# Optimization experiments

Hardware: AMD Instinct MI355X
Metric: run time of the kernel (lower is better)

## Reference

```python
import jax, jax.numpy as jnp
import numpy as np

E = 1_000_000
C_IN = 11
H = 64
N_LAYERS = 4
LN_EPS = 1e-5


def setup_inputs() -> dict:
    key = jax.random.key(0)
    ks = jax.random.split(key, 12)
    x = jax.random.normal(ks[0], (E, C_IN), dtype=jnp.float32)
    neighbors = jax.random.randint(ks[1], (E, 4), 0, E)
    s0 = 1.0 / np.sqrt(5 * C_IN)
    s1 = 1.0 / np.sqrt(5 * H)
    w0 = jax.random.uniform(ks[2], (5 * C_IN, H), jnp.float32, -s0, s0)
    b0 = jax.random.uniform(ks[3], (H,), jnp.float32, -s0, s0)
    w_rest = jax.random.uniform(ks[4], (N_LAYERS - 1, 5 * H, H), jnp.float32, -s1, s1)
    b_rest = jax.random.uniform(ks[5], (N_LAYERS - 1, H), jnp.float32, -s1, s1)
    ln_g = jnp.ones((N_LAYERS, H), jnp.float32)
    ln_b = jnp.zeros((N_LAYERS, H), jnp.float32)
    sc1 = 1.0 / np.sqrt(H)
    sc2 = 1.0 / np.sqrt(H // 2)
    cw1 = jax.random.uniform(ks[6], (H, H // 2), jnp.float32, -sc1, sc1)
    cb1 = jax.random.uniform(ks[7], (H // 2,), jnp.float32, -sc1, sc1)
    cw2 = jax.random.uniform(ks[8], (H // 2, 1), jnp.float32, -sc2, sc2)
    cb2 = jax.random.uniform(ks[9], (1,), jnp.float32, -sc2, sc2)
    return {"x": x, "neighbors": neighbors, "w0": w0, "b0": b0,
            "w_rest": w_rest, "b_rest": b_rest, "ln_g": ln_g, "ln_b": ln_b,
            "cw1": cw1, "cb1": cb1, "cw2": cw2, "cb2": cb2}


def _mesh_conv(x, neighbors, W, b):
    # Gather 4-ring neighbor features: [E,4,C]
    n = x[neighbors]
    a, bb, c, d = n[:, 0], n[:, 1], n[:, 2], n[:, 3]
    # Symmetric MeshCNN features -> 5*C, then linear projection.
    feats = jnp.concatenate([x, jnp.abs(a - c), a + c, jnp.abs(bb - d), bb + d], axis=-1)
    return feats @ W + b


def _layernorm(h, g, b):
    mu = jnp.mean(h, axis=-1, keepdims=True)
    var = jnp.var(h, axis=-1, keepdims=True)
    return (h - mu) * jax.lax.rsqrt(var + LN_EPS) * g + b


def reference(x, neighbors, w0, b0, w_rest, b_rest, ln_g, ln_b, cw1, cb1, cw2, cb2):
    # Layer 0 (no residual; dropout is identity in eval mode)
    h = jax.nn.relu(_layernorm(_mesh_conv(x, neighbors, w0, b0), ln_g[0], ln_b[0]))
    x = h
    for i in range(1, N_LAYERS):
        h = _mesh_conv(x, neighbors, w_rest[i - 1], b_rest[i - 1])
        h = jax.nn.relu(_layernorm(h, ln_g[i], ln_b[i]))
        x = h + x  # residual from layer 2 onward (shapes match)
    z = jax.nn.relu(x @ cw1 + cb1)
    logits = (z @ cw2 + cb2).squeeze(-1)
    return logits
```

## Files before the change

kernel.cpp:

```cpp
#include <hip/hip_runtime.h>
#include <hip/hip_bf16.h>
#include <math.h>

#define E_EDGES 1000000
#define LN_EPS  1e-5f

typedef unsigned short u16;
typedef __bf16 bf16x8 __attribute__((ext_vector_type(8)));
typedef float  f32x16 __attribute__((ext_vector_type(16)));

__device__ __forceinline__ float lo2f(unsigned d) {
    union { unsigned u; float f; } v; v.u = d << 16; return v.f;
}
__device__ __forceinline__ float hi2f(unsigned d) {
    union { unsigned u; float f; } v; v.u = d & 0xffff0000u; return v.f;
}
__device__ __forceinline__ unsigned pk2(float lo, float hi) {
    __hip_bfloat162 h = __float22bfloat162_rn(make_float2(lo, hi));
    unsigned r; __builtin_memcpy(&r, &h, 4); return r;
}

__global__ __launch_bounds__(256) void wconv_kernel(
    const float* __restrict__ wr, const float* __restrict__ w0,
    u16* __restrict__ wf)
{
    const int s = blockIdx.x * 256 + threadIdx.x;
    const int l    = s & 63;
    const int nt   = (s >> 6) & 1;
    const int col  = nt * 32 + (l & 31);
    const int half = l >> 5;
    uint4 pk;
    if (s < 3 * 2560) {
        const int L  = s / 2560;
        const int sl = s % 2560;
        const int kb = (sl >> 7) * 16 + half * 8;
        const float* W = wr + L * 320 * 64;
        pk.x = pk2(W[(kb+0)*64+col], W[(kb+1)*64+col]);
        pk.y = pk2(W[(kb+2)*64+col], W[(kb+3)*64+col]);
        pk.z = pk2(W[(kb+4)*64+col], W[(kb+5)*64+col]);
        pk.w = pk2(W[(kb+6)*64+col], W[(kb+7)*64+col]);
    } else {
        const int sl = s - 3 * 2560;
        const int kb = (sl >> 7) * 16 + half * 8;
        float v[8];
        #pragma unroll
        for (int p = 0; p < 8; ++p) v[p] = (kb + p < 55) ? w0[(kb+p)*64 + col] : 0.f;
        pk.x = pk2(v[0],v[1]); pk.y = pk2(v[2],v[3]);
        pk.z = pk2(v[4],v[5]); pk.w = pk2(v[6],v[7]);
    }
    *(uint4*)&wf[(size_t)s * 8] = pk;
}

__global__ __launch_bounds__(256, 4) void layer_mfma(
    const u16* __restrict__ xin, const int* __restrict__ nbr,
    const u16* __restrict__ wf, const float* __restrict__ bias,
    const float* __restrict__ lng, const float* __restrict__ lnb,
    u16* __restrict__ xout)
{
    __shared__ u16 afrag[2 * 20 * 64 * 8];
    const int t  = threadIdx.x;
    const int l  = t & 63;
    const int wv = t >> 6;
    const int e0 = blockIdx.x * 64;

    {
        const int el = t >> 2;
        const int cq = t & 3;
        const size_t e = (size_t)(e0 + el);
        const int4 n = *(const int4*)(nbr + 4 * e);
        const u16* xr = xin + e * 64           + cq * 16;
        const u16* ar = xin + (size_t)n.x * 64 + cq * 16;
        const u16* br = xin + (size_t)n.y * 64 + cq * 16;
        const u16* cr = xin + (size_t)n.z * 64 + cq * 16;
        const u16* dr = xin + (size_t)n.w * 64 + cq * 16;
        const uint4 xv0 = *(const uint4*)(xr);     const uint4 xv1 = *(const uint4*)(xr + 8);
        const uint4 av0 = *(const uint4*)(ar);     const uint4 av1 = *(const uint4*)(ar + 8);
        const uint4 bv0 = *(const uint4*)(br);     const uint4 bv1 = *(const uint4*)(br + 8);
        const uint4 cv0 = *(const uint4*)(cr);     const uint4 cv1 = *(const uint4*)(cr + 8);
        const uint4 dv0 = *(const uint4*)(dr);     const uint4 dv1 = *(const uint4*)(dr + 8);
        const int mt    = el >> 5;
        const int lane0 = el & 31;
        u16* abase = afrag + (size_t)mt * (20 * 64 * 8);
        #pragma unroll
        for (int w8 = 0; w8 < 2; ++w8) {
            const uint4 xv = w8 ? xv1 : xv0;
            const uint4 av = w8 ? av1 : av0;
            const uint4 bv = w8 ? bv1 : bv0;
            const uint4 cv = w8 ? cv1 : cv0;
            const uint4 dv = w8 ? dv1 : dv0;
            const int ldst = lane0 + 32 * w8;
            uint4 g1, g2, g3, g4;
            const unsigned* ap = (const unsigned*)&av;
            const unsigned* bp = (const unsigned*)&bv;
            const unsigned* cp = (const unsigned*)&cv;
            const unsigned* dp = (const unsigned*)&dv;
            unsigned* g1p = (unsigned*)&g1; unsigned* g2p = (unsigned*)&g2;
            unsigned* g3p = (unsigned*)&g3; unsigned* g4p = (unsigned*)&g4;
            #pragma unroll
            for (int i = 0; i < 4; ++i) {
                const float a0 = lo2f(ap[i]), a1 = hi2f(ap[i]);
                const float c0 = lo2f(cp[i]), c1 = hi2f(cp[i]);
                g1p[i] = pk2(fabsf(a0 - c0), fabsf(a1 - c1));
                g2p[i] = pk2(a0 + c0, a1 + c1);
                const float b0 = lo2f(bp[i]), b1 = hi2f(bp[i]);
                const float d0 = lo2f(dp[i]), d1 = hi2f(dp[i]);
                g3p[i] = pk2(fabsf(b0 - d0), fabsf(b1 - d1));
                g4p[i] = pk2(b0 + d0, b1 + d1);
            }
            *(uint4*)(abase + (size_t)(((0*4 + cq) * 64) + ldst) * 8) = xv;
            *(uint4*)(abase + (size_t)(((1*4 + cq) * 64) + ldst) * 8) = g1;
            *(uint4*)(abase + (size_t)(((2*4 + cq) * 64) + ldst) * 8) = g2;
            *(uint4*)(abase + (size_t)(((3*4 + cq) * 64) + ldst) * 8) = g3;
            *(uint4*)(abase + (size_t)(((4*4 + cq) * 64) + ldst) * 8) = g4;
        }
    }
    __syncthreads();

    const int mt = wv >> 1, nt = wv & 1;
    f32x16 acc = {};
    const u16* ab = afrag + (size_t)mt * (20 * 64 * 8) + l * 8;
    const u16* bb = wf + (size_t)(nt * 64 + l) * 8;
    #pragma unroll
    for (int ks = 0; ks < 20; ++ks) {
        const bf16x8 a8 = *(const bf16x8*)(ab + ks * 512);
        const bf16x8 b8 = *(const bf16x8*)(bb + ks * 1024);
        acc = __builtin_amdgcn_mfma_f32_32x32x16_bf16(a8, b8, acc, 0, 0, 0);
    }
    __syncthreads();

    float* ebuf = (float*)afrag;
    {
        const int col  = nt * 32 + (l & 31);
        const int quad = l >> 5;
        const float bc = bias[col];
        #pragma unroll
        for (int r = 0; r < 16; ++r) {
            const int row = mt * 32 + (r & 3) + 8 * (r >> 2) + 4 * quad;
            ebuf[row * 68 + col] = acc[r] + bc;
        }
    }
    __syncthreads();

    {
        const int el = t >> 2, q = t & 3;
        const float* rp = ebuf + el * 68 + q * 16;
        float v[16];
        float s = 0.f, qs = 0.f;
        #pragma unroll
        for (int i = 0; i < 16; ++i) { v[i] = rp[i]; s += v[i]; qs += v[i] * v[i]; }
        s  += __shfl_xor(s, 1);  s  += __shfl_xor(s, 2);
        qs += __shfl_xor(qs, 1); qs += __shfl_xor(qs, 2);
        const float mu   = s * (1.f / 64.f);
        const float var  = qs * (1.f / 64.f) - mu * mu;
        const float rinv = rsqrtf(var + LN_EPS);
        const size_t e   = (size_t)(e0 + el);
        const u16* resp  = xin + e * 64 + q * 16;
        u16* outp        = xout + e * 64 + q * 16;
        #pragma unroll
        for (int h = 0; h < 2; ++h) {
            const uint4 res = *(const uint4*)(resp + h * 8);
            const unsigned* rr = (const unsigned*)&res;
            uint4 o; unsigned* op = (unsigned*)&o;
            #pragma unroll
            for (int i = 0; i < 4; ++i) {
                const int ci = q * 16 + h * 8 + i * 2;
                const float y0 = fmaxf(fmaf((v[h*8 + i*2]     - mu) * rinv, lng[ci],     lnb[ci]),     0.f) + lo2f(rr[i]);
                const float y1 = fmaxf(fmaf((v[h*8 + i*2 + 1] - mu) * rinv, lng[ci + 1], lnb[ci + 1]), 0.f) + hi2f(rr[i]);
                op[i] = pk2(y0, y1);
            }
            *(uint4*)(outp + h * 8) = o;
        }
    }
}

__global__ __launch_bounds__(256) void layer0_mfma(
    const float* __restrict__ x, const int* __restrict__ nbr,
    const u16* __restrict__ wf0, const float* __restrict__ bias,
    const float* __restrict__ lng, const float* __restrict__ lnb,
    u16* __restrict__ xout)
{
    __shared__ float smem[128 * 68];
    u16* afrag = (u16*)smem;
    const int t  = threadIdx.x;
    const int l  = t & 63;
    const int wv = t >> 6;
    const int e0 = blockIdx.x * 128;

    {
        const int el = t & 127;
        const int h  = t >> 7;
        const size_t e  = (size_t)(e0 + el);
        const size_t ec = e < E_EDGES ? e : (size_t)(E_EDGES - 1);
        const int4 n = *(const int4*)(nbr + 4 * ec);
        const float* xr = x + ec * 11;
        const float* ar = x + (size_t)n.x * 11;
        const float* br = x + (size_t)n.y * 11;
        const float* cr = x + (size_t)n.z * 11;
        const float* dr = x + (size_t)n.w * 11;
        float f[32];
        if (h == 0) {
            #pragma unroll
            for (int i = 0; i < 11; ++i) f[i] = xr[i];
            #pragma unroll
            for (int i = 0; i < 11; ++i) { const float a = ar[i], c = cr[i];
                f[11 + i] = fabsf(a - c); if (i < 10) f[22 + i] = a + c; }
        } else {
            f[0] = ar[10] + cr[10];
            #pragma unroll
            for (int i = 0; i < 11; ++i) { const float b = br[i], d = dr[i];
                f[1 + i] = fabsf(b - d); f[12 + i] = b + d; }
            #pragma unroll
            for (int i = 23; i < 32; ++i) f[i] = 0.f;
        }
        const int mt    = el >> 5;
        const int lane0 = el & 31;
        u16* abase = afrag + (size_t)mt * (4 * 64 * 8);
        #pragma unroll
        for (int s8 = 0; s8 < 4; ++s8) {
            const int k0   = h * 32 + s8 * 8;
            const int ks   = k0 >> 4;
            const int half = (k0 >> 3) & 1;
            uint4 pk;
            pk.x = pk2(f[s8*8+0], f[s8*8+1]);
            pk.y = pk2(f[s8*8+2], f[s8*8+3]);
            pk.z = pk2(f[s8*8+4], f[s8*8+5]);
            pk.w = pk2(f[s8*8+6], f[s8*8+7]);
            *(uint4*)(abase + (size_t)(ks * 64 + lane0 + 32 * half) * 8) = pk;
        }
    }
    __syncthreads();

    f32x16 acc0 = {}, acc1 = {};
    const u16* ab = afrag + (size_t)wv * (4 * 64 * 8) + l * 8;
    #pragma unroll
    for (int ks = 0; ks < 4; ++ks) {
        const bf16x8 a8 = *(const bf16x8*)(ab + ks * 512);
        const bf16x8 b0 = *(const bf16x8*)(wf0 + (size_t)((ks*2    ) * 64 + l) * 8);
        const bf16x8 b1 = *(const bf16x8*)(wf0 + (size_t)((ks*2 + 1) * 64 + l) * 8);
        acc0 = __builtin_amdgcn_mfma_f32_32x32x16_bf16(a8, b0, acc0, 0, 0, 0);
        acc1 = __builtin_amdgcn_mfma_f32_32x32x16_bf16(a8, b1, acc1, 0, 0, 0);
    }
    __syncthreads();

    float* ebuf = smem;
    {
        const int col0 = l & 31;
        const int quad = l >> 5;
        const float bc0 = bias[col0];
        const float bc1 = bias[col0 + 32];
        #pragma unroll
        for (int r = 0; r < 16; ++r) {
            const int row = wv * 32 + (r & 3) + 8 * (r >> 2) + 4 * quad;
            ebuf[row * 68 + col0]      = acc0[r] + bc0;
            ebuf[row * 68 + col0 + 32] = acc1[r] + bc1;
        }
    }
    __syncthreads();

    {
        const int el = t >> 1, hf = t & 1;
        const float* rp = ebuf + el * 68 + hf * 32;
        float v[32];
        float s = 0.f, q = 0.f;
        #pragma unroll
        for (int i = 0; i < 32; ++i) { v[i] = rp[i]; s += v[i]; q += v[i] * v[i]; }
        s += __shfl_xor(s, 1); q += __shfl_xor(q, 1);
        const float mu   = s * (1.f / 64.f);
        const float var  = q * (1.f / 64.f) - mu * mu;
        const float rinv = rsqrtf(var + LN_EPS);
        const size_t e = (size_t)(e0 + el);
        if (e < E_EDGES) {
            u16* outp       = xout + e * 64 + hf * 32;
            const float* gp = lng + hf * 32;
            const float* bp = lnb + hf * 32;
            #pragma unroll
            for (int w8 = 0; w8 < 4; ++w8) {
                uint4 o; unsigned* op = (unsigned*)&o;
                #pragma unroll
                for (int i = 0; i < 4; ++i) {
                    const int ci = w8 * 8 + i * 2;
                    const float y0 = fmaxf(fmaf((v[ci]   - mu) * rinv, gp[ci],   bp[ci]),   0.f);
                    const float y1 = fmaxf(fmaf((v[ci+1] - mu) * rinv, gp[ci+1], bp[ci+1]), 0.f);
                    op[i] = pk2(y0, y1);
                }
                *(uint4*)(outp + w8 * 8) = o;
            }
        }
    }
}

__global__ __launch_bounds__(256) void head_mfma(
    const u16* __restrict__ xin,
    const float* __restrict__ cw1, const float* __restrict__ cb1,
    const float* __restrict__ cw2, const float* __restrict__ cb2,
    float* __restrict__ out)
{
    const int t    = threadIdx.x;
    const int l    = t & 63;
    const int wv   = t >> 6;
    const int col  = l & 31;
    const int half = l >> 5;

    bf16x8 bf[4];
    #pragma unroll
    for (int ks = 0; ks < 4; ++ks) {
        const int kb = ks * 16 + half * 8;
        uint4 pk;
        pk.x = pk2(cw1[(kb+0)*32 + col], cw1[(kb+1)*32 + col]);
        pk.y = pk2(cw1[(kb+2)*32 + col], cw1[(kb+3)*32 + col]);
        pk.z = pk2(cw1[(kb+4)*32 + col], cw1[(kb+5)*32 + col]);
        pk.w = pk2(cw1[(kb+6)*32 + col], cw1[(kb+7)*32 + col]);
        __builtin_memcpy(&bf[ks], &pk, 16);
    }
    const float bc = cb1[col];
    const float w2 = cw2[col];
    const float b2 = cb2[0];

    const int nwaves = gridDim.x * 4;
    for (int tile = blockIdx.x * 4 + wv; tile < E_EDGES / 32; tile += nwaves) {
        const size_t e0 = (size_t)tile * 32;
        const u16* xb = xin + (e0 + col) * 64 + half * 8;
        f32x16 acc = {};
        #pragma unroll
        for (int ks = 0; ks < 4; ++ks) {
            const bf16x8 a8 = *(const bf16x8*)(xb + ks * 16);
            acc = __builtin_amdgcn_mfma_f32_32x32x16_bf16(a8, bf[ks], acc, 0, 0, 0);
        }
        float sums[16];
        #pragma unroll
        for (int r = 0; r < 16; ++r) {
            float z = fmaxf(acc[r] + bc, 0.f) * w2;
            z += __shfl_xor(z, 1); z += __shfl_xor(z, 2); z += __shfl_xor(z, 4);
            z += __shfl_xor(z, 8); z += __shfl_xor(z, 16);
            sums[r] = z;
        }
        if (col == 0) {
            #pragma unroll
            for (int r = 0; r < 16; ++r) {
                const int row = (r & 3) + 8 * (r >> 2) + 4 * half;
                out[e0 + row] = sums[r] + b2;
            }
        }
    }
}

extern "C" void kernel_launch(void* const* d_in, const int* in_sizes, int n_in,
                              void* d_out, int out_size, void* d_ws, size_t ws_size,
                              hipStream_t stream)
{
    (void)in_sizes; (void)n_in; (void)out_size; (void)ws_size;
    const float* x   = (const float*)d_in[0];
    const int*   nbr = (const int*)d_in[1];
    const float* w0  = (const float*)d_in[2];
    const float* b0  = (const float*)d_in[3];
    const float* wr  = (const float*)d_in[4];
    const float* br  = (const float*)d_in[5];
    const float* lg  = (const float*)d_in[6];
    const float* lb  = (const float*)d_in[7];
    const float* cw1 = (const float*)d_in[8];
    const float* cb1 = (const float*)d_in[9];
    const float* cw2 = (const float*)d_in[10];
    const float* cb2 = (const float*)d_in[11];
    float* out = (float*)d_out;

    u16* xa = (u16*)d_ws;
    u16* xb = xa + (size_t)E_EDGES * 64;
    u16* wfrag = (u16*)d_out;

    const dim3 blk(256);

    wconv_kernel<<<dim3(32), blk, 0, stream>>>(wr, w0, wfrag);
    layer0_mfma<<<dim3((E_EDGES + 127) / 128), blk, 0, stream>>>(x, nbr, wfrag + 3*20480, b0, lg, lb, xa);
    layer_mfma<<<dim3(E_EDGES / 64), blk, 0, stream>>>(xa, nbr, wfrag,           br,        lg + 64,  lb + 64,  xb);
    layer_mfma<<<dim3(E_EDGES / 64), blk, 0, stream>>>(xb, nbr, wfrag + 20480,   br + 64,   lg + 128, lb + 128, xa);
    layer_mfma<<<dim3(E_EDGES / 64), blk, 0, stream>>>(xa, nbr, wfrag + 40960,   br + 128,  lg + 192, lb + 192, xb);
    head_mfma<<<dim3(2048), blk, 0, stream>>>(xb, cw1, cb1, cw2, cb2, out);
}
```

Baseline: 695.2 us.

## Swizzle LDS A-fragments, reuse residual registers, restructure layer0 and head kernels

In the hidden layers, the A-fragment LDS writes and reads are XOR-swizzled to reduce bank conflicts. The residual now comes from the self-row registers already loaded during the gather rather than a second global read, and abs is done as a sign-mask on the packed bf16. Layer0 moves to 64-edge blocks with 4 threads per edge, a 2x2 wave/MFMA split and a higher occupancy hint. The head kernel becomes one tile per wave with an LDS row reduction in place of the 5-step shuffle chain and grid-stride loop. These are several independent changes at once, and the extra LDS traffic in the head may offset some of the gain.

```diff
diff --git a/kernel.cpp b/kernel.cpp
--- a/kernel.cpp
+++ b/kernel.cpp
@@ -62,10 +62,11 @@
     const int l  = t & 63;
     const int wv = t >> 6;
     const int e0 = blockIdx.x * 64;
-
-    {
-        const int el = t >> 2;
-        const int cq = t & 3;
+    const int el = t >> 2;
+    const int cq = t & 3;
+
+    uint4 xv0, xv1;
+    {
         const size_t e = (size_t)(e0 + el);
         const int4 n = *(const int4*)(nbr + 4 * e);
         const u16* xr = xin + e * 64           + cq * 16;
@@ -73,14 +74,14 @@
         const u16* br = xin + (size_t)n.y * 64 + cq * 16;
         const u16* cr = xin + (size_t)n.z * 64 + cq * 16;
         const u16* dr = xin + (size_t)n.w * 64 + cq * 16;
-        const uint4 xv0 = *(const uint4*)(xr);     const uint4 xv1 = *(const uint4*)(xr + 8);
+        xv0 = *(const uint4*)(xr);                 xv1 = *(const uint4*)(xr + 8);
         const uint4 av0 = *(const uint4*)(ar);     const uint4 av1 = *(const uint4*)(ar + 8);
         const uint4 bv0 = *(const uint4*)(br);     const uint4 bv1 = *(const uint4*)(br + 8);
         const uint4 cv0 = *(const uint4*)(cr);     const uint4 cv1 = *(const uint4*)(cr + 8);
         const uint4 dv0 = *(const uint4*)(dr);     const uint4 dv1 = *(const uint4*)(dr + 8);
-        const int mt    = el >> 5;
+        const int mt_g  = el >> 5;
         const int lane0 = el & 31;
-        u16* abase = afrag + (size_t)mt * (20 * 64 * 8);
+        u16* abase = afrag + (size_t)mt_g * (20 * 64 * 8);
         #pragma unroll
         for (int w8 = 0; w8 < 2; ++w8) {
             const uint4 xv = w8 ? xv1 : xv0;
@@ -88,7 +89,7 @@
             const uint4 bv = w8 ? bv1 : bv0;
             const uint4 cv = w8 ? cv1 : cv0;
             const uint4 dv = w8 ? dv1 : dv0;
-            const int ldst = lane0 + 32 * w8;
+            const int gsw = (lane0 + 32 * w8) ^ cq;
             uint4 g1, g2, g3, g4;
             const unsigned* ap = (const unsigned*)&av;
             const unsigned* bp = (const unsigned*)&bv;
@@ -100,29 +101,29 @@
             for (int i = 0; i < 4; ++i) {
                 const float a0 = lo2f(ap[i]), a1 = hi2f(ap[i]);
                 const float c0 = lo2f(cp[i]), c1 = hi2f(cp[i]);
-                g1p[i] = pk2(fabsf(a0 - c0), fabsf(a1 - c1));
+                g1p[i] = pk2(a0 - c0, a1 - c1) & 0x7FFF7FFFu;
                 g2p[i] = pk2(a0 + c0, a1 + c1);
                 const float b0 = lo2f(bp[i]), b1 = hi2f(bp[i]);
                 const float d0 = lo2f(dp[i]), d1 = hi2f(dp[i]);
-                g3p[i] = pk2(fabsf(b0 - d0), fabsf(b1 - d1));
+                g3p[i] = pk2(b0 - d0, b1 - d1) & 0x7FFF7FFFu;
                 g4p[i] = pk2(b0 + d0, b1 + d1);
             }
-            *(uint4*)(abase + (size_t)(((0*4 + cq) * 64) + ldst) * 8) = xv;
-            *(uint4*)(abase + (size_t)(((1*4 + cq) * 64) + ldst) * 8) = g1;
-            *(uint4*)(abase + (size_t)(((2*4 + cq) * 64) + ldst) * 8) = g2;
-            *(uint4*)(abase + (size_t)(((3*4 + cq) * 64) + ldst) * 8) = g3;
-            *(uint4*)(abase + (size_t)(((4*4 + cq) * 64) + ldst) * 8) = g4;
+            *(uint4*)(abase + (size_t)(((0*4 + cq) * 64) + gsw) * 8) = xv;
+            *(uint4*)(abase + (size_t)(((1*4 + cq) * 64) + gsw) * 8) = g1;
+            *(uint4*)(abase + (size_t)(((2*4 + cq) * 64) + gsw) * 8) = g2;
+            *(uint4*)(abase + (size_t)(((3*4 + cq) * 64) + gsw) * 8) = g3;
+            *(uint4*)(abase + (size_t)(((4*4 + cq) * 64) + gsw) * 8) = g4;
         }
     }
     __syncthreads();
 
     const int mt = wv >> 1, nt = wv & 1;
     f32x16 acc = {};
-    const u16* ab = afrag + (size_t)mt * (20 * 64 * 8) + l * 8;
+    const u16* ab = afrag + (size_t)mt * (20 * 512);
     const u16* bb = wf + (size_t)(nt * 64 + l) * 8;
     #pragma unroll
     for (int ks = 0; ks < 20; ++ks) {
-        const bf16x8 a8 = *(const bf16x8*)(ab + ks * 512);
+        const bf16x8 a8 = *(const bf16x8*)(ab + (size_t)(ks * 64 + (l ^ (ks & 3))) * 8);
         const bf16x8 b8 = *(const bf16x8*)(bb + ks * 1024);
         acc = __builtin_amdgcn_mfma_f32_32x32x16_bf16(a8, b8, acc, 0, 0, 0);
     }
@@ -142,8 +143,7 @@
     __syncthreads();
 
     {
-        const int el = t >> 2, q = t & 3;
-        const float* rp = ebuf + el * 68 + q * 16;
+        const float* rp = ebuf + el * 68 + cq * 16;
         float v[16];
         float s = 0.f, qs = 0.f;
         #pragma unroll
@@ -154,16 +154,15 @@
         const float var  = qs * (1.f / 64.f) - mu * mu;
         const float rinv = rsqrtf(var + LN_EPS);
         const size_t e   = (size_t)(e0 + el);
-        const u16* resp  = xin + e * 64 + q * 16;
-        u16* outp        = xout + e * 64 + q * 16;
+        u16* outp        = xout + e * 64 + cq * 16;
         #pragma unroll
         for (int h = 0; h < 2; ++h) {
-            const uint4 res = *(const uint4*)(resp + h * 8);
+            const uint4 res = h ? xv1 : xv0;
             const unsigned* rr = (const unsigned*)&res;
             uint4 o; unsigned* op = (unsigned*)&o;
             #pragma unroll
             for (int i = 0; i < 4; ++i) {
-                const int ci = q * 16 + h * 8 + i * 2;
+                const int ci = cq * 16 + h * 8 + i * 2;
                 const float y0 = fmaxf(fmaf((v[h*8 + i*2]     - mu) * rinv, lng[ci],     lnb[ci]),     0.f) + lo2f(rr[i]);
                 const float y1 = fmaxf(fmaf((v[h*8 + i*2 + 1] - mu) * rinv, lng[ci + 1], lnb[ci + 1]), 0.f) + hi2f(rr[i]);
                 op[i] = pk2(y0, y1);
@@ -173,118 +172,116 @@
     }
 }
 
-__global__ __launch_bounds__(256) void layer0_mfma(
+__global__ __launch_bounds__(256, 6) void layer0_mfma(
     const float* __restrict__ x, const int* __restrict__ nbr,
     const u16* __restrict__ wf0, const float* __restrict__ bias,
     const float* __restrict__ lng, const float* __restrict__ lnb,
     u16* __restrict__ xout)
 {
-    __shared__ float smem[128 * 68];
+    __shared__ float smem[64 * 68];
     u16* afrag = (u16*)smem;
     const int t  = threadIdx.x;
     const int l  = t & 63;
     const int wv = t >> 6;
-    const int e0 = blockIdx.x * 128;
-
-    {
-        const int el = t & 127;
-        const int h  = t >> 7;
-        const size_t e  = (size_t)(e0 + el);
-        const size_t ec = e < E_EDGES ? e : (size_t)(E_EDGES - 1);
-        const int4 n = *(const int4*)(nbr + 4 * ec);
-        const float* xr = x + ec * 11;
+    const int e0 = blockIdx.x * 64;
+    const int el = t >> 2, cq = t & 3;
+
+    {
+        const size_t e = (size_t)(e0 + el);
+        const int4 n = *(const int4*)(nbr + 4 * e);
+        const float* xr = x + e * 11;
         const float* ar = x + (size_t)n.x * 11;
         const float* br = x + (size_t)n.y * 11;
         const float* cr = x + (size_t)n.z * 11;
         const float* dr = x + (size_t)n.w * 11;
-        float f[32];
-        if (h == 0) {
+        float f[16];
+        if (cq == 0) {
             #pragma unroll
             for (int i = 0; i < 11; ++i) f[i] = xr[i];
             #pragma unroll
-            for (int i = 0; i < 11; ++i) { const float a = ar[i], c = cr[i];
-                f[11 + i] = fabsf(a - c); if (i < 10) f[22 + i] = a + c; }
+            for (int i = 0; i < 5; ++i) f[11 + i] = fabsf(ar[i] - cr[i]);
+        } else if (cq == 1) {
+            #pragma unroll
+            for (int i = 0; i < 6; ++i) f[i] = fabsf(ar[5 + i] - cr[5 + i]);
+            #pragma unroll
+            for (int i = 0; i < 10; ++i) f[6 + i] = ar[i] + cr[i];
+        } else if (cq == 2) {
+            f[0] = ar[10] + cr[10];
+            #pragma unroll
+            for (int i = 0; i < 11; ++i) f[1 + i] = fabsf(br[i] - dr[i]);
+            #pragma unroll
+            for (int i = 0; i < 4; ++i) f[12 + i] = br[i] + dr[i];
         } else {
-            f[0] = ar[10] + cr[10];
-            #pragma unroll
-            for (int i = 0; i < 11; ++i) { const float b = br[i], d = dr[i];
-                f[1 + i] = fabsf(b - d); f[12 + i] = b + d; }
-            #pragma unroll
-            for (int i = 23; i < 32; ++i) f[i] = 0.f;
-        }
-        const int mt    = el >> 5;
+            #pragma unroll
+            for (int i = 0; i < 7; ++i) f[i] = br[4 + i] + dr[4 + i];
+            #pragma unroll
+            for (int i = 7; i < 16; ++i) f[i] = 0.f;
+        }
+        const int mt_g  = el >> 5;
         const int lane0 = el & 31;
-        u16* abase = afrag + (size_t)mt * (4 * 64 * 8);
-        #pragma unroll
-        for (int s8 = 0; s8 < 4; ++s8) {
-            const int k0   = h * 32 + s8 * 8;
-            const int ks   = k0 >> 4;
-            const int half = (k0 >> 3) & 1;
+        u16* abase = afrag + (size_t)mt_g * (4 * 64 * 8);
+        #pragma unroll
+        for (int hh = 0; hh < 2; ++hh) {
             uint4 pk;
-            pk.x = pk2(f[s8*8+0], f[s8*8+1]);
-            pk.y = pk2(f[s8*8+2], f[s8*8+3]);
-            pk.z = pk2(f[s8*8+4], f[s8*8+5]);
-            pk.w = pk2(f[s8*8+6], f[s8*8+7]);
-            *(uint4*)(abase + (size_t)(ks * 64 + lane0 + 32 * half) * 8) = pk;
-        }
-    }
-    __syncthreads();
-
-    f32x16 acc0 = {}, acc1 = {};
-    const u16* ab = afrag + (size_t)wv * (4 * 64 * 8) + l * 8;
+            pk.x = pk2(f[hh*8+0], f[hh*8+1]);
+            pk.y = pk2(f[hh*8+2], f[hh*8+3]);
+            pk.z = pk2(f[hh*8+4], f[hh*8+5]);
+            pk.w = pk2(f[hh*8+6], f[hh*8+7]);
+            const int gsw = (lane0 + 32 * hh) ^ cq;
+            *(uint4*)(abase + (size_t)(cq * 64 + gsw) * 8) = pk;
+        }
+    }
+    __syncthreads();
+
+    const int mt = wv >> 1, nt = wv & 1;
+    f32x16 acc = {};
+    const u16* ab = afrag + (size_t)mt * (4 * 512);
+    const u16* bb = wf0 + (size_t)(nt * 64 + l) * 8;
     #pragma unroll
     for (int ks = 0; ks < 4; ++ks) {
-        const bf16x8 a8 = *(const bf16x8*)(ab + ks * 512);
-        const bf16x8 b0 = *(const bf16x8*)(wf0 + (size_t)((ks*2    ) * 64 + l) * 8);
-        const bf16x8 b1 = *(const bf16x8*)(wf0 + (size_t)((ks*2 + 1) * 64 + l) * 8);
-        acc0 = __builtin_amdgcn_mfma_f32_32x32x16_bf16(a8, b0, acc0, 0, 0, 0);
-        acc1 = __builtin_amdgcn_mfma_f32_32x32x16_bf16(a8, b1, acc1, 0, 0, 0);
+        const bf16x8 a8 = *(const bf16x8*)(ab + (size_t)(ks * 64 + (l ^ ks)) * 8);
+        const bf16x8 b8 = *(const bf16x8*)(bb + ks * 1024);
+        acc = __builtin_amdgcn_mfma_f32_32x32x16_bf16(a8, b8, acc, 0, 0, 0);
     }
     __syncthreads();
 
     float* ebuf = smem;
     {
-        const int col0 = l & 31;
+        const int col  = nt * 32 + (l & 31);
         const int quad = l >> 5;
-        const float bc0 = bias[col0];
-        const float bc1 = bias[col0 + 32];
+        const float bc = bias[col];
         #pragma unroll
         for (int r = 0; r < 16; ++r) {
-            const int row = wv * 32 + (r & 3) + 8 * (r >> 2) + 4 * quad;
-            ebuf[row * 68 + col0]      = acc0[r] + bc0;
-            ebuf[row * 68 + col0 + 32] = acc1[r] + bc1;
-        }
-    }
-    __syncthreads();
-
-    {
-        const int el = t >> 1, hf = t & 1;
-        const float* rp = ebuf + el * 68 + hf * 32;
-        float v[32];
-        float s = 0.f, q = 0.f;
-        #pragma unroll
-        for (int i = 0; i < 32; ++i) { v[i] = rp[i]; s += v[i]; q += v[i] * v[i]; }
-        s += __shfl_xor(s, 1); q += __shfl_xor(q, 1);
+            const int row = mt * 32 + (r & 3) + 8 * (r >> 2) + 4 * quad;
+            ebuf[row * 68 + col] = acc[r] + bc;
+        }
+    }
+    __syncthreads();
+
+    {
+        const float* rp = ebuf + el * 68 + cq * 16;
+        float v[16];
+        float s = 0.f, qs = 0.f;
+        #pragma unroll
+        for (int i = 0; i < 16; ++i) { v[i] = rp[i]; s += v[i]; qs += v[i] * v[i]; }
+        s  += __shfl_xor(s, 1);  s  += __shfl_xor(s, 2);
+        qs += __shfl_xor(qs, 1); qs += __shfl_xor(qs, 2);
         const float mu   = s * (1.f / 64.f);
-        const float var  = q * (1.f / 64.f) - mu * mu;
+        const float var  = qs * (1.f / 64.f) - mu * mu;
         const float rinv = rsqrtf(var + LN_EPS);
-        const size_t e = (size_t)(e0 + el);
-        if (e < E_EDGES) {
-            u16* outp       = xout + e * 64 + hf * 32;
-            const float* gp = lng + hf * 32;
-            const float* bp = lnb + hf * 32;
-            #pragma unroll
-            for (int w8 = 0; w8 < 4; ++w8) {
-                uint4 o; unsigned* op = (unsigned*)&o;
-                #pragma unroll
-                for (int i = 0; i < 4; ++i) {
-                    const int ci = w8 * 8 + i * 2;
-                    const float y0 = fmaxf(fmaf((v[ci]   - mu) * rinv, gp[ci],   bp[ci]),   0.f);
-                    const float y1 = fmaxf(fmaf((v[ci+1] - mu) * rinv, gp[ci+1], bp[ci+1]), 0.f);
-                    op[i] = pk2(y0, y1);
-                }
-                *(uint4*)(outp + w8 * 8) = o;
+        const size_t e   = (size_t)(e0 + el);
+        u16* outp        = xout + e * 64 + cq * 16;
+        #pragma unroll
+        for (int h = 0; h < 2; ++h) {
+            uint4 o; unsigned* op = (unsigned*)&o;
+            #pragma unroll
+            for (int i = 0; i < 4; ++i) {
+                const int ci = cq * 16 + h * 8 + i * 2;
+                const float y0 = fmaxf(fmaf((v[h*8 + i*2]     - mu) * rinv, lng[ci],     lnb[ci]),     0.f);
+                const float y1 = fmaxf(fmaf((v[h*8 + i*2 + 1] - mu) * rinv, lng[ci + 1], lnb[ci + 1]), 0.f);
+                op[i] = pk2(y0, y1);
             }
+            *(uint4*)(outp + h * 8) = o;
         }
     }
 }
@@ -295,6 +292,7 @@
     const float* __restrict__ cw2, const float* __restrict__ cb2,
     float* __restrict__ out)
 {
+    __shared__ float hbuf[4][32 * 33];
     const int t    = threadIdx.x;
     const int l    = t & 63;
     const int wv   = t >> 6;
@@ -316,32 +314,31 @@
     const float w2 = cw2[col];
     const float b2 = cb2[0];
 
-    const int nwaves = gridDim.x * 4;
-    for (int tile = blockIdx.x * 4 + wv; tile < E_EDGES / 32; tile += nwaves) {
-        const size_t e0 = (size_t)tile * 32;
-        const u16* xb = xin + (e0 + col) * 64 + half * 8;
-        f32x16 acc = {};
-        #pragma unroll
-        for (int ks = 0; ks < 4; ++ks) {
-            const bf16x8 a8 = *(const bf16x8*)(xb + ks * 16);
-            acc = __builtin_amdgcn_mfma_f32_32x32x16_bf16(a8, bf[ks], acc, 0, 0, 0);
-        }
-        float sums[16];
-        #pragma unroll
-        for (int r = 0; r < 16; ++r) {
-            float z = fmaxf(acc[r] + bc, 0.f) * w2;
-            z += __shfl_xor(z, 1); z += __shfl_xor(z, 2); z += __shfl_xor(z, 4);
-            z += __shfl_xor(z, 8); z += __shfl_xor(z, 16);
-            sums[r] = z;
-        }
-        if (col == 0) {
-            #pragma unroll
-            for (int r = 0; r < 16; ++r) {
-                const int row = (r & 3) + 8 * (r >> 2) + 4 * half;
-                out[e0 + row] = sums[r] + b2;
-            }
-        }
-    }
+    int tile = blockIdx.x * 4 + wv;
+    const int valid = tile < (E_EDGES / 32);
+    if (!valid) tile = E_EDGES / 32 - 1;
+    const size_t e0 = (size_t)tile * 32;
+    const u16* xb = xin + (e0 + col) * 64 + half * 8;
+    f32x16 acc = {};
+    #pragma unroll
+    for (int ks = 0; ks < 4; ++ks) {
+        const bf16x8 a8 = *(const bf16x8*)(xb + ks * 16);
+        acc = __builtin_amdgcn_mfma_f32_32x32x16_bf16(a8, bf[ks], acc, 0, 0, 0);
+    }
+    float* hb = hbuf[wv];
+    #pragma unroll
+    for (int r = 0; r < 16; ++r) {
+        const int row = (r & 3) + 8 * (r >> 2) + 4 * half;
+        hb[row * 33 + col] = fmaxf(acc[r] + bc, 0.f) * w2;
+    }
+    __syncthreads();
+    const int row2 = l >> 1, part = l & 1;
+    const float* rp = hb + row2 * 33 + part * 16;
+    float s = 0.f;
+    #pragma unroll
+    for (int i = 0; i < 16; ++i) s += rp[i];
+    s += __shfl_xor(s, 1);
+    if (valid && part == 0) out[e0 + row2] = s + b2;
 }
 
 extern "C" void kernel_launch(void* const* d_in, const int* in_sizes, int n_in,
@@ -370,9 +367,9 @@
     const dim3 blk(256);
 
     wconv_kernel<<<dim3(32), blk, 0, stream>>>(wr, w0, wfrag);
-    layer0_mfma<<<dim3((E_EDGES + 127) / 128), blk, 0, stream>>>(x, nbr, wfrag + 3*20480, b0, lg, lb, xa);
+    layer0_mfma<<<dim3(E_EDGES / 64), blk, 0, stream>>>(x, nbr, wfrag + 3*20480, b0, lg, lb, xa);
     layer_mfma<<<dim3(E_EDGES / 64), blk, 0, stream>>>(xa, nbr, wfrag,           br,        lg + 64,  lb + 64,  xb);
     layer_mfma<<<dim3(E_EDGES / 64), blk, 0, stream>>>(xb, nbr, wfrag + 20480,   br + 64,   lg + 128, lb + 128, xa);
     layer_mfma<<<dim3(E_EDGES / 64), blk, 0, stream>>>(xa, nbr, wfrag + 40960,   br + 128,  lg + 192, lb + 192, xb);
-    head_mfma<<<dim3(2048), blk, 0, stream>>>(xb, cw1, cb1, cw2, cb2, out);
-}
+    head_mfma<<<dim3((E_EDGES / 32 + 3) / 4), blk, 0, stream>>>(xb, cw1, cb1, cw2, cb2, out);
+}
```

After: 684.3 us. Within noise of the previous version (-1.6%).
